# Kernel optimization log

Measured on AMD Instinct MI355X. Metric: run time of the kernel, lower is better.

The kernel has to match this reference:

```python
import jax, jax.numpy as jnp
import numpy as np
from jax import lax

B_, L_, D_ = 4, 3136, 256
DH, DS, DR = 256, 16, 16  # d_inner//2, d_state, dt_rank (ceil(256/16))


def _ln(x, g, b):
    m = x.mean(-1, keepdims=True)
    v = ((x - m) ** 2).mean(-1, keepdims=True)
    return (x - m) * lax.rsqrt(v + 1e-5) * g + b


def _dwconv_same(x, w):
    # x: (B, C, L), w: (C, 1, K) depthwise, padding='same', no bias
    return lax.conv_general_dilated(x, w, (1,), 'SAME',
        dimension_numbers=('NCH', 'OIH', 'NCH'), feature_group_count=x.shape[1])


def _selective_scan(u, delta, A, Bm, Cm, Dp, delta_bias):
    # u, delta: (b, d, l); A: (d, n); Bm, Cm: (b, n, l)
    delta = jax.nn.softplus(delta + delta_bias[None, :, None])
    dA = jnp.exp(jnp.einsum('bdl,dn->lbdn', delta, A))          # (l,b,d,n)
    dBu = jnp.einsum('bdl,bnl,bdl->lbdn', delta, Bm, u)          # (l,b,d,n)
    C_l = jnp.transpose(Cm, (2, 0, 1))                           # (l,b,n)
    h0 = jnp.zeros(dA.shape[1:], u.dtype)

    def step(h, inp):
        dA_t, dBu_t, C_t = inp
        h = dA_t * h + dBu_t
        return h, jnp.einsum('bdn,bn->bd', h, C_t)

    _, ys = lax.scan(step, h0, (dA, dBu, C_l))                   # ys: (l,b,d)
    return jnp.transpose(ys, (1, 2, 0)) + u * Dp[None, :, None]


def _mamba(x, in_proj_w, conv_x_w, conv_z_w, x_proj_w, dt_proj_w, dt_proj_b, A_log, Dp, out_proj_w):
    xz = jnp.einsum('bld,ed->bel', x, in_proj_w)                 # (b, 2*DH, l)
    xb, zb = xz[:, :DH], xz[:, DH:]
    xb = jax.nn.silu(_dwconv_same(xb, conv_x_w))
    zb = jax.nn.silu(_dwconv_same(zb, conv_z_w))
    x_dbl = jnp.einsum('bdl,ed->ble', xb, x_proj_w)              # (b, l, DR+2*DS)
    dt, Bm, Cm = x_dbl[..., :DR], x_dbl[..., DR:DR + DS], x_dbl[..., DR + DS:]
    delta = jnp.einsum('blr,dr->bdl', dt, dt_proj_w)             # (b, DH, l)
    Bm = jnp.transpose(Bm, (0, 2, 1))                            # (b, DS, l)
    Cm = jnp.transpose(Cm, (0, 2, 1))
    A = -jnp.exp(A_log)
    y = _selective_scan(xb, delta, A, Bm, Cm, Dp, dt_proj_b)     # (b, DH, l)
    y = jnp.concatenate([y, zb], axis=1)                         # (b, 2*DH, l)
    return jnp.einsum('bel,de->bld', y, out_proj_w)


def _block(x, ln1_g, ln1_b, ln2_g, ln2_b, in_proj_w, conv_x_w, conv_z_w,
           x_proj_w, dt_proj_w, dt_proj_b, A_log, Dp, out_proj_w,
           mlp_w1, mlp_b1, mlp_w2, mlp_b2):
    x = x + _mamba(_ln(x, ln1_g, ln1_b), in_proj_w, conv_x_w, conv_z_w,
                   x_proj_w, dt_proj_w, dt_proj_b, A_log, Dp, out_proj_w)
    h = _ln(x, ln2_g, ln2_b)
    h = jax.nn.gelu(jnp.einsum('bld,hd->blh', h, mlp_w1) + mlp_b1, approximate=False)
    return x + (jnp.einsum('blh,dh->bld', h, mlp_w2) + mlp_b2)


def setup_inputs() -> dict:
    key = jax.random.key(0)
    ks = jax.random.split(key, 12)
    f = lambda k, s, sc=0.02: jax.random.normal(k, s, dtype=jnp.float32) * sc
    dt = jnp.exp(jax.random.uniform(ks[9], (DH,), dtype=jnp.float32)
                 * (np.log(0.1) - np.log(0.001)) + np.log(0.001))
    dt = jnp.clip(dt, 1e-4)
    inv_dt = dt + jnp.log(-jnp.expm1(-dt))
    return {
        'x': jax.random.normal(ks[0], (B_, L_, D_), dtype=jnp.float32),
        'ln1_g': jnp.ones((D_,), jnp.float32), 'ln1_b': jnp.zeros((D_,), jnp.float32),
        'ln2_g': jnp.ones((D_,), jnp.float32), 'ln2_b': jnp.zeros((D_,), jnp.float32),
        'in_proj_w': f(ks[1], (2 * DH, D_)),
        'conv_x_w': f(ks[2], (DH, 1, 3), 0.1),
        'conv_z_w': f(ks[3], (DH, 1, 3), 0.1),
        'x_proj_w': f(ks[4], (DR + 2 * DS, DH)),
        'dt_proj_w': f(ks[5], (DH, DR), DR ** -0.5),
        'dt_proj_b': inv_dt,
        'A_log': jnp.log(jnp.tile(jnp.arange(1, DS + 1, dtype=jnp.float32)[None, :], (DH, 1))),
        'Dp': jnp.ones((DH,), jnp.float32),
        'out_proj_w': f(ks[6], (D_, 2 * DH)),
        'mlp_w1': f(ks[7], (4 * D_, D_)), 'mlp_b1': jnp.zeros((4 * D_,), jnp.float32),
        'mlp_w2': f(ks[8], (D_, 4 * D_)), 'mlp_b2': jnp.zeros((D_,), jnp.float32),
    }


def reference(x, ln1_g, ln1_b, ln2_g, ln2_b, in_proj_w, conv_x_w, conv_z_w,
              x_proj_w, dt_proj_w, dt_proj_b, A_log, Dp, out_proj_w,
              mlp_w1, mlp_b1, mlp_w2, mlp_b2):
    return _block(x, ln1_g, ln1_b, ln2_g, ln2_b, in_proj_w, conv_x_w, conv_z_w,
                  x_proj_w, dt_proj_w, dt_proj_b, A_log, Dp, out_proj_w,
                  mlp_w1, mlp_b1, mlp_w2, mlp_b2)
```

## Files before the change

kernel.cpp:

```cpp
#include <hip/hip_runtime.h>
#include <hip/hip_bf16.h>

#define B_ 4
#define L_ 3136
#define D_ 256
#define NCH 49
#define LCH 64
#define M_ (B_*L_)

__device__ __forceinline__ float bf2f(unsigned short u) {
    union { unsigned int i; float f; } v; v.i = ((unsigned int)u) << 16; return v.f;
}
__device__ __forceinline__ unsigned short f2bs(float f) {
    __hip_bfloat16 h = __float2bfloat16(f);
    return *(unsigned short*)&h;
}
__device__ __forceinline__ float ldw(const void* p, size_t i, bool bf) {
    return bf ? bf2f(((const unsigned short*)p)[i]) : ((const float*)p)[i];
}
__device__ __forceinline__ void cvt4(ushort4 a, float* o) {
    o[0] = bf2f(a.x); o[1] = bf2f(a.y); o[2] = bf2f(a.z); o[3] = bf2f(a.w);
}
__device__ __forceinline__ void cvt8g(const unsigned short* p, bool v, float* o) {
    if (v) {
        ushort4 a = *(const ushort4*)p;
        ushort4 b = *(const ushort4*)(p + 4);
        cvt4(a, o); cvt4(b, o + 4);
    } else {
        #pragma unroll
        for (int i = 0; i < 8; ++i) o[i] = 0.f;
    }
}
__device__ __forceinline__ float dpp_add_xor1(float x) {
    int m = __builtin_amdgcn_update_dpp(0, __float_as_int(x), 0xB1, 0xF, 0xF, true);
    return x + __int_as_float(m);
}
__device__ __forceinline__ float dpp_add_xor2(float x) {
    int m = __builtin_amdgcn_update_dpp(0, __float_as_int(x), 0x4E, 0xF, 0xF, true);
    return x + __int_as_float(m);
}

__global__ __launch_bounds__(256) void detect_kernel(
    const unsigned int* __restrict__ xw, int* __restrict__ flag)
{
    int t = threadIdx.x; int cnt = 0;
    for (int i = t; i < 2048; i += 256) {
        unsigned int lo = xw[i] & 0xFFFFu;
        unsigned int e = (lo >> 7) & 0xFFu;
        if (e >= 0x58u && e <= 0x97u) cnt++;
    }
    #pragma unroll
    for (int o = 32; o > 0; o >>= 1) cnt += __shfl_down(cnt, o);
    __shared__ int sred[4];
    if ((t & 63) == 0) sred[t >> 6] = cnt;
    __syncthreads();
    if (t == 0) flag[0] = (sred[0] + sred[1] + sred[2] + sred[3] > 1024) ? 1 : 0;
}

__global__ __launch_bounds__(256) void ln_kernel(
    const void* __restrict__ xin, int inmode,
    const void* __restrict__ g, const void* __restrict__ bsh,
    unsigned short* __restrict__ out, const int* __restrict__ flagp)
{
    const bool wbf = (*flagp != 0);
    const bool inbf = (inmode < 0) ? wbf : true;
    int row = blockIdx.x * 4 + (threadIdx.x >> 6);
    int lane = threadIdx.x & 63;
    size_t idx = (size_t)row * 256 + lane * 4;
    float v[4];
    if (inbf) {
        ushort4 a = *(const ushort4*)((const unsigned short*)xin + idx);
        cvt4(a, v);
    } else {
        float4 a = *(const float4*)((const float*)xin + idx);
        v[0] = a.x; v[1] = a.y; v[2] = a.z; v[3] = a.w;
    }
    float s = v[0] + v[1] + v[2] + v[3];
    float s2 = v[0]*v[0] + v[1]*v[1] + v[2]*v[2] + v[3]*v[3];
    #pragma unroll
    for (int o = 32; o > 0; o >>= 1) { s += __shfl_xor(s, o); s2 += __shfl_xor(s2, o); }
    float mean = s * (1.f / 256.f);
    float var  = s2 * (1.f / 256.f) - mean * mean;
    float rs = rsqrtf(var + 1e-5f);
    ushort4 o;
    o.x = f2bs((v[0] - mean) * rs * ldw(g, lane*4+0, wbf) + ldw(bsh, lane*4+0, wbf));
    o.y = f2bs((v[1] - mean) * rs * ldw(g, lane*4+1, wbf) + ldw(bsh, lane*4+1, wbf));
    o.z = f2bs((v[2] - mean) * rs * ldw(g, lane*4+2, wbf) + ldw(bsh, lane*4+2, wbf));
    o.w = f2bs((v[3] - mean) * rs * ldw(g, lane*4+3, wbf) + ldw(bsh, lane*4+3, wbf));
    *(ushort4*)(out + idx) = o;
}

enum { EPI_NONE = 0, EPI_SP = 1, EPI_RES = 2, EPI_GELU = 3, EPI_OUT = 4 };

typedef __attribute__((ext_vector_type(8))) short bf16x8;
typedef __attribute__((ext_vector_type(4))) float f32x4;

__device__ __forceinline__ void gload_lds16(const void* g, void* l) {
    __builtin_amdgcn_global_load_lds(
        (const __attribute__((address_space(1))) unsigned int*)g,
        (__attribute__((address_space(3))) unsigned int*)l, 16, 0, 0);
}

template<int EPI>
__global__ __launch_bounds__(256) void mgemm_kernel(
    const unsigned short* __restrict__ A, const unsigned short* __restrict__ A2, int Ksplit,
    const void* __restrict__ W, void* __restrict__ Cout,
    int N, int K, int lda, int ldc,
    const void* __restrict__ bias, const void* __restrict__ resb,
    const unsigned short* __restrict__ resf, const int* __restrict__ flagp)
{
    const bool wbf = (*flagp != 0);
    __shared__ unsigned short As[2][64][64];
    __shared__ unsigned short Ws[2][64][64];
    const int tid = threadIdx.x;

    const int nwg = gridDim.x * gridDim.y;
    int bid = blockIdx.y * gridDim.x + blockIdx.x;
    int wgid = ((nwg & 7) == 0) ? ((bid & 7) * (nwg >> 3) + (bid >> 3)) : bid;
    const int bx = wgid % gridDim.x;
    const int by = wgid / gridDim.x;
    const int bm = by * 64, bn = bx * 64;

    const int l = tid & 63, wid = tid >> 6;
    const int wr = wid >> 1, wc = wid & 1;
    const int lr = l & 15;
    const int lq = l >> 4;
    const int srow = tid >> 3;
    const int sblk = ((tid & 7) ^ (srow & 7)) * 8;
    const int dcol = (tid & 7) * 8;

    f32x4 acc[2][2] = {};
    const int NT = K >> 6;

    auto stage = [&](int buf, int k0s) {
        const unsigned short* Ab; int kc;
        if (k0s < Ksplit) { Ab = A;  kc = k0s; }
        else              { Ab = A2; kc = k0s - Ksplit; }
        gload_lds16(Ab + (size_t)(bm + srow) * lda + kc + sblk,      &As[buf][srow][dcol]);
        gload_lds16(Ab + (size_t)(bm + 32 + srow) * lda + kc + sblk, &As[buf][32 + srow][dcol]);
        if (wbf) {
            const unsigned short* Wb = (const unsigned short*)W;
            gload_lds16(Wb + (size_t)(bn + srow) * K + k0s + sblk,      &Ws[buf][srow][dcol]);
            gload_lds16(Wb + (size_t)(bn + 32 + srow) * K + k0s + sblk, &Ws[buf][32 + srow][dcol]);
        } else {
            const float* Wf = (const float*)W;
            #pragma unroll
            for (int h = 0; h < 2; ++h) {
                int row = h * 32 + srow;
                const float* p = Wf + (size_t)(bn + row) * K + k0s + (tid & 7) * 8;
                float4 w0 = *(const float4*)p;
                float4 w1 = *(const float4*)(p + 4);
                ushort4 o0, o1;
                o0.x = f2bs(w0.x); o0.y = f2bs(w0.y); o0.z = f2bs(w0.z); o0.w = f2bs(w0.w);
                o1.x = f2bs(w1.x); o1.y = f2bs(w1.y); o1.z = f2bs(w1.z); o1.w = f2bs(w1.w);
                *(ushort4*)&Ws[buf][row][sblk]     = o0;
                *(ushort4*)&Ws[buf][row][sblk + 4] = o1;
            }
        }
    };

    stage(0, 0);
    asm volatile("s_waitcnt vmcnt(0)" ::: "memory");
    __syncthreads();

    int cur = 0;
    for (int kt = 0; kt < NT; ++kt) {
        if (kt + 1 < NT) stage(cur ^ 1, (kt + 1) << 6);

        bf16x8 af[2][2], bfr[2][2];
        #pragma unroll
        for (int i = 0; i < 2; ++i) {
            #pragma unroll
            for (int ks = 0; ks < 2; ++ks) {
                int ca = ((ks * 4 + lq) ^ (lr & 7)) * 8;
                af[i][ks]  = *(const bf16x8*)&As[cur][wr * 32 + i * 16 + lr][ca];
                bfr[i][ks] = *(const bf16x8*)&Ws[cur][wc * 32 + i * 16 + lr][ca];
            }
        }
        #pragma unroll
        for (int ks = 0; ks < 2; ++ks)
            #pragma unroll
            for (int i = 0; i < 2; ++i)
                #pragma unroll
                for (int j = 0; j < 2; ++j)
                    acc[i][j] = __builtin_amdgcn_mfma_f32_16x16x32_bf16(af[i][ks], bfr[j][ks], acc[i][j], 0, 0, 0);

        if (kt + 1 < NT) {
            asm volatile("s_waitcnt vmcnt(0)" ::: "memory");
            __syncthreads();
            cur ^= 1;
        }
    }

    #pragma unroll
    for (int i = 0; i < 2; ++i) {
        #pragma unroll
        for (int j = 0; j < 2; ++j) {
            const int col = bn + wc * 32 + j * 16 + lr;
            #pragma unroll
            for (int e = 0; e < 4; ++e) {
                const int row = bm + wr * 32 + i * 16 + lq * 4 + e;
                float t = acc[i][j][e];
                if (EPI == EPI_RES) {
                    t += ldw(resb, (size_t)row * 256 + col, wbf);
                } else if (EPI == EPI_GELU) {
                    t += ldw(bias, col, wbf);
                    t = 0.5f * t * (1.f + erff(t * 0.70710678118654752f));
                } else if (EPI == EPI_OUT) {
                    t += ldw(bias, col, wbf) + bf2f(resf[(size_t)row * 256 + col]);
                }
                if (EPI == EPI_OUT && !wbf) {
                    ((float*)Cout)[(size_t)row * ldc + col] = t;
                } else {
                    ((unsigned short*)Cout)[(size_t)row * ldc + col] = f2bs(t);
                }
            }
        }
    }
}

__global__ __launch_bounds__(256) void xproj_kernel(
    const unsigned short* __restrict__ A, const void* __restrict__ W,
    float* __restrict__ Cout, const int* __restrict__ flagp)
{
    const bool wbf = (*flagp != 0);
    __shared__ unsigned short As[2][64][64];
    __shared__ unsigned short Ws[2][64][64];
    const int tid = threadIdx.x;
    const int bm = blockIdx.y * 64;

    const int l = tid & 63, wid = tid >> 6;
    const int wr = wid >> 1, wc = wid & 1;
    const int lr = l & 15, lq = l >> 4;
    const int srow = tid >> 3;
    const int sblk = ((tid & 7) ^ (srow & 7)) * 8;
    const int dcol = (tid & 7) * 8;

    {
        ushort4 zz4; zz4.x = 0; zz4.y = 0; zz4.z = 0; zz4.w = 0;
        int buf = tid >> 7, rr = 48 + ((tid >> 3) & 15), cc = (tid & 7) * 8;
        *(ushort4*)&Ws[buf][rr][cc] = zz4;
        *(ushort4*)&Ws[buf][rr][cc + 4] = zz4;
    }
    __syncthreads();

    f32x4 acc[2][2] = {};

    auto stage = [&](int buf, int k0s) {
        gload_lds16(A + (size_t)(bm + srow) * 256 + k0s + sblk,      &As[buf][srow][dcol]);
        gload_lds16(A + (size_t)(bm + 32 + srow) * 256 + k0s + sblk, &As[buf][32 + srow][dcol]);
        if (wbf) {
            const unsigned short* Wb = (const unsigned short*)W;
            gload_lds16(Wb + (size_t)srow * 256 + k0s + sblk, &Ws[buf][srow][dcol]);
            if (srow < 16)
                gload_lds16(Wb + (size_t)(32 + srow) * 256 + k0s + sblk, &Ws[buf][32 + srow][dcol]);
        } else {
            const float* Wf = (const float*)W;
            #pragma unroll
            for (int h = 0; h < 2; ++h) {
                int row = h * 32 + srow;
                if (row < 48) {
                    const float* p = Wf + (size_t)row * 256 + k0s + (tid & 7) * 8;
                    float4 w0 = *(const float4*)p;
                    float4 w1 = *(const float4*)(p + 4);
                    ushort4 o0, o1;
                    o0.x = f2bs(w0.x); o0.y = f2bs(w0.y); o0.z = f2bs(w0.z); o0.w = f2bs(w0.w);
                    o1.x = f2bs(w1.x); o1.y = f2bs(w1.y); o1.z = f2bs(w1.z); o1.w = f2bs(w1.w);
                    *(ushort4*)&Ws[buf][row][sblk]     = o0;
                    *(ushort4*)&Ws[buf][row][sblk + 4] = o1;
                }
            }
        }
    };

    stage(0, 0);
    asm volatile("s_waitcnt vmcnt(0)" ::: "memory");
    __syncthreads();

    int cur = 0;
    for (int kt = 0; kt < 4; ++kt) {
        if (kt + 1 < 4) stage(cur ^ 1, (kt + 1) << 6);
        bf16x8 af[2][2], bfr[2][2];
        #pragma unroll
        for (int i = 0; i < 2; ++i) {
            #pragma unroll
            for (int ks = 0; ks < 2; ++ks) {
                int ca = ((ks * 4 + lq) ^ (lr & 7)) * 8;
                af[i][ks]  = *(const bf16x8*)&As[cur][wr * 32 + i * 16 + lr][ca];
                bfr[i][ks] = *(const bf16x8*)&Ws[cur][wc * 32 + i * 16 + lr][ca];
            }
        }
        #pragma unroll
        for (int ks = 0; ks < 2; ++ks)
            #pragma unroll
            for (int i = 0; i < 2; ++i)
                #pragma unroll
                for (int j = 0; j < 2; ++j)
                    acc[i][j] = __builtin_amdgcn_mfma_f32_16x16x32_bf16(af[i][ks], bfr[j][ks], acc[i][j], 0, 0, 0);
        if (kt + 1 < 4) {
            asm volatile("s_waitcnt vmcnt(0)" ::: "memory");
            __syncthreads();
            cur ^= 1;
        }
    }

    #pragma unroll
    for (int i = 0; i < 2; ++i) {
        #pragma unroll
        for (int j = 0; j < 2; ++j) {
            const int col = wc * 32 + j * 16 + lr;
            if (col < 48) {
                #pragma unroll
                for (int e = 0; e < 4; ++e) {
                    const int row = bm + wr * 32 + i * 16 + lq * 4 + e;
                    Cout[(size_t)row * 48 + col] = acc[i][j][e];
                }
            }
        }
    }
}

__global__ __launch_bounds__(256) void dtgemm_kernel(
    const float* __restrict__ Axd, const void* __restrict__ W,
    unsigned short* __restrict__ Cout, const void* __restrict__ bias,
    const int* __restrict__ flagp)
{
    const bool wbf = (*flagp != 0);
    __shared__ unsigned short Ah[64][16];
    __shared__ unsigned short Al[64][16];
    __shared__ unsigned short Wb[64][16];
    const int tid = threadIdx.x;
    const int nwg = gridDim.x * gridDim.y;
    int bid = blockIdx.y * gridDim.x + blockIdx.x;
    int wgid = ((nwg & 7) == 0) ? ((bid & 7) * (nwg >> 3) + (bid >> 3)) : bid;
    const int bx = wgid % gridDim.x, by = wgid / gridDim.x;
    const int bm = by * 64, bn = bx * 64;

    {
        int rr = tid >> 2, cc = (tid & 3) * 4;
        float4 v = *(const float4*)(Axd + (size_t)(bm + rr) * 48 + cc);
        float vv[4] = {v.x, v.y, v.z, v.w};
        ushort4 hi4, lo4;
        unsigned short* hp = (unsigned short*)&hi4;
        unsigned short* lp = (unsigned short*)&lo4;
        #pragma unroll
        for (int j = 0; j < 4; ++j) {
            unsigned short h = f2bs(vv[j]);
            hp[j] = h;
            lp[j] = f2bs(vv[j] - bf2f(h));
        }
        *(ushort4*)&Ah[rr][cc] = hi4;
        *(ushort4*)&Al[rr][cc] = lo4;
        ushort4 wb4;
        unsigned short* wp = (unsigned short*)&wb4;
        if (wbf) {
            wb4 = *(const ushort4*)((const unsigned short*)W + (size_t)(bn + rr) * 16 + cc);
        } else {
            float4 wv = *(const float4*)((const float*)W + (size_t)(bn + rr) * 16 + cc);
            wp[0] = f2bs(wv.x); wp[1] = f2bs(wv.y); wp[2] = f2bs(wv.z); wp[3] = f2bs(wv.w);
        }
        *(ushort4*)&Wb[rr][cc] = wb4;
    }
    __syncthreads();

    const int l = tid & 63, wid = tid >> 6;
    const int wr = wid >> 1, wc = wid & 1;
    const int lr = l & 15, lq = l >> 4;

    f32x4 acc[2][2] = {};
    bf16x8 ah[2], al8[2], wb8[2];
    #pragma unroll
    for (int i = 0; i < 2; ++i) { ah[i] = bf16x8{}; al8[i] = bf16x8{}; wb8[i] = bf16x8{}; }
    if (lq < 2) {
        #pragma unroll
        for (int i = 0; i < 2; ++i) {
            ah[i]  = *(const bf16x8*)&Ah[wr * 32 + i * 16 + lr][lq * 8];
            al8[i] = *(const bf16x8*)&Al[wr * 32 + i * 16 + lr][lq * 8];
            wb8[i] = *(const bf16x8*)&Wb[wc * 32 + i * 16 + lr][lq * 8];
        }
    }
    #pragma unroll
    for (int i = 0; i < 2; ++i)
        #pragma unroll
        for (int j = 0; j < 2; ++j) {
            acc[i][j] = __builtin_amdgcn_mfma_f32_16x16x32_bf16(ah[i],  wb8[j], acc[i][j], 0, 0, 0);
            acc[i][j] = __builtin_amdgcn_mfma_f32_16x16x32_bf16(al8[i], wb8[j], acc[i][j], 0, 0, 0);
        }

    #pragma unroll
    for (int i = 0; i < 2; ++i) {
        #pragma unroll
        for (int j = 0; j < 2; ++j) {
            const int col = bn + wc * 32 + j * 16 + lr;
            #pragma unroll
            for (int e = 0; e < 4; ++e) {
                const int row = bm + wr * 32 + i * 16 + lq * 4 + e;
                float t = acc[i][j][e] + ldw(bias, col, wbf);
                t = (t > 20.f) ? t : log1pf(__expf(t));
                Cout[(size_t)row * 256 + col] = f2bs(t);
            }
        }
    }
}

__global__ __launch_bounds__(256) void conv_silu_kernel(
    const unsigned short* __restrict__ xz,
    const void* __restrict__ wx, const void* __restrict__ wz,
    unsigned short* __restrict__ u, unsigned short* __restrict__ z,
    const int* __restrict__ flagp)
{
    const bool wbf = (*flagp != 0);
    int sub = threadIdx.x >> 5;
    int cb = (threadIdx.x & 31) * 8;
    int bl = blockIdx.x * 8 + sub;
    int l = bl % L_;
    const unsigned short* r = xz + (size_t)bl * 512;
    bool hasm = (l > 0), hasp = (l < L_ - 1);

    float wxa[24], wza[24];
    if (wbf) {
        const unsigned short* px = (const unsigned short*)wx + 3 * cb;
        const unsigned short* pz = (const unsigned short*)wz + 3 * cb;
        #pragma unroll
        for (int t = 0; t < 3; ++t) {
            cvt4(*(const ushort4*)(px + t * 8), &wxa[t * 8]);
            cvt4(*(const ushort4*)(px + t * 8 + 4), &wxa[t * 8 + 4]);
            cvt4(*(const ushort4*)(pz + t * 8), &wza[t * 8]);
            cvt4(*(const ushort4*)(pz + t * 8 + 4), &wza[t * 8 + 4]);
        }
    } else {
        const float* px = (const float*)wx + 3 * cb;
        const float* pz = (const float*)wz + 3 * cb;
        #pragma unroll
        for (int t = 0; t < 6; ++t) {
            *(float4*)&wxa[t * 4] = *(const float4*)(px + t * 4);
            *(float4*)&wza[t * 4] = *(const float4*)(pz + t * 4);
        }
    }

    float xm[8], xc[8], xp[8];
    cvt8g(r + cb - 512, hasm, xm);
    cvt8g(r + cb,       true, xc);
    cvt8g(r + cb + 512, hasp, xp);
    ushort4 o0, o1;
    {
        unsigned short* op = (unsigned short*)&o0;
        unsigned short* op1 = (unsigned short*)&o1;
        #pragma unroll
        for (int j = 0; j < 8; ++j) {
            float v = xm[j] * wxa[3 * j] + xc[j] * wxa[3 * j + 1] + xp[j] * wxa[3 * j + 2];
            v = v / (1.f + __expf(-v));
            if (j < 4) op[j] = f2bs(v); else op1[j - 4] = f2bs(v);
        }
    }
    *(ushort4*)(u + (size_t)bl * 256 + cb) = o0;
    *(ushort4*)(u + (size_t)bl * 256 + cb + 4) = o1;

    cvt8g(r + cb - 256,  hasm, xm);
    cvt8g(r + 256 + cb,  true, xc);
    cvt8g(r + 768 + cb,  hasp, xp);
    {
        unsigned short* op = (unsigned short*)&o0;
        unsigned short* op1 = (unsigned short*)&o1;
        #pragma unroll
        for (int j = 0; j < 8; ++j) {
            float v = xm[j] * wza[3 * j] + xc[j] * wza[3 * j + 1] + xp[j] * wza[3 * j + 2];
            v = v / (1.f + __expf(-v));
            if (j < 4) op[j] = f2bs(v); else op1[j - 4] = f2bs(v);
        }
    }
    *(ushort4*)(z + (size_t)bl * 256 + cb) = o0;
    *(ushort4*)(z + (size_t)bl * 256 + cb + 4) = o1;
}

__global__ __launch_bounds__(256) void scan_a_kernel(
    const unsigned short* __restrict__ delta, const unsigned short* __restrict__ u,
    const float* __restrict__ xdbl, const void* __restrict__ A_log,
    float* __restrict__ hend, float* __restrict__ dsum, const int* __restrict__ flagp)
{
    const bool wbf = (*flagp != 0);
    int blk = blockIdx.x;
    int b = blk / (NCH * 16);
    int rem = blk % (NCH * 16);
    int c = rem / 16, db = rem % 16;

    __shared__ unsigned int sduT[16][68];
    __shared__ float sBT[16][68];

    const unsigned short* dp = delta + (size_t)b * L_ * 256;
    const unsigned short* up = u     + (size_t)b * L_ * 256;
    const float* xd = xdbl + (size_t)b * L_ * 48;

    int r = threadIdx.x >> 2, q = (threadIdx.x & 3) * 4;
    int lrow = c * 64 + r;
    {
        ushort4 dv = *(const ushort4*)(dp + (size_t)lrow * 256 + db * 16 + q);
        ushort4 uv = *(const ushort4*)(up + (size_t)lrow * 256 + db * 16 + q);
        sduT[q + 0][r] = (unsigned)dv.x | ((unsigned)uv.x << 16);
        sduT[q + 1][r] = (unsigned)dv.y | ((unsigned)uv.y << 16);
        sduT[q + 2][r] = (unsigned)dv.z | ((unsigned)uv.z << 16);
        sduT[q + 3][r] = (unsigned)dv.w | ((unsigned)uv.w << 16);
        float4 Bv = *(const float4*)(xd + (size_t)lrow * 48 + 16 + q);
        sBT[q + 0][r] = Bv.x; sBT[q + 1][r] = Bv.y;
        sBT[q + 2][r] = Bv.z; sBT[q + 3][r] = Bv.w;
    }
    __syncthreads();

    int g = threadIdx.x >> 4, n = threadIdx.x & 15;
    int d = db * 16 + g;
    float An2 = -__expf(ldw(A_log, d * 16 + n, wbf)) * 1.44269504088896f;
    float h = 0.f, s = 0.f;
    #pragma unroll 4
    for (int tb = 0; tb < 16; ++tb) {
        uint4 du4 = *(const uint4*)&sduT[g][tb * 4];
        float4 B4 = *(const float4*)&sBT[n][tb * 4];
        #pragma unroll
        for (int j = 0; j < 4; ++j) {
            unsigned du = (j == 0) ? du4.x : (j == 1) ? du4.y : (j == 2) ? du4.z : du4.w;
            float Bn = (j == 0) ? B4.x : (j == 1) ? B4.y : (j == 2) ? B4.z : B4.w;
            float ds = __uint_as_float(du << 16);
            float ut = __uint_as_float(du & 0xFFFF0000u);
            float e = exp2f(ds * An2);
            h = fmaf(e, h, ds * ut * Bn);
            s += ds;
        }
    }
    size_t pair = (size_t)b * 256 + d;
    hend[(pair * NCH + c) * 16 + n] = h;
    if (n == 0) dsum[pair * NCH + c] = s;
}

__global__ __launch_bounds__(64) void scan_b_kernel(
    const void* __restrict__ A_log, float* __restrict__ hend,
    const float* __restrict__ dsum, const int* __restrict__ flagp)
{
    const bool wbf = (*flagp != 0);
    int gid = blockIdx.x * 64 + threadIdx.x;
    int pair = gid >> 4, n = gid & 15;
    int d = pair & 255;
    float An = -__expf(ldw(A_log, d * 16 + n, wbf));
    float H = 0.f;
    #pragma unroll 1
    for (int c0 = 0; c0 < NCH; c0 += 7) {
        float he[7], dd[7];
        #pragma unroll
        for (int j = 0; j < 7; ++j) {
            he[j] = hend[((size_t)pair * NCH + c0 + j) * 16 + n];
            dd[j] = dsum[(size_t)pair * NCH + c0 + j];
        }
        #pragma unroll
        for (int j = 0; j < 7; ++j) {
            hend[((size_t)pair * NCH + c0 + j) * 16 + n] = H;
            H = __expf(An * dd[j]) * H + he[j];
        }
    }
}

__global__ __launch_bounds__(256) void scan_c_kernel(
    const unsigned short* __restrict__ delta, const unsigned short* __restrict__ u,
    const float* __restrict__ xdbl, const void* __restrict__ A_log,
    const void* __restrict__ Dp, const float* __restrict__ hinit,
    unsigned short* __restrict__ y, const int* __restrict__ flagp)
{
    const bool wbf = (*flagp != 0);
    int blk = blockIdx.x;
    int b = blk / (NCH * 16);
    int rem = blk % (NCH * 16);
    int c = rem / 16, db = rem % 16;

    __shared__ unsigned int sduT[16][68];
    __shared__ float sBCT[16][132];
    __shared__ float sypT[16][4][68];
    __shared__ unsigned short sy[64][16];

    const unsigned short* dp = delta + (size_t)b * L_ * 256;
    const unsigned short* up = u     + (size_t)b * L_ * 256;
    const float* xd = xdbl + (size_t)b * L_ * 48;

    int r = threadIdx.x >> 2, q = (threadIdx.x & 3) * 4;
    int lrow = c * 64 + r;
    {
        ushort4 dv = *(const ushort4*)(dp + (size_t)lrow * 256 + db * 16 + q);
        ushort4 uv = *(const ushort4*)(up + (size_t)lrow * 256 + db * 16 + q);
        sduT[q + 0][r] = (unsigned)dv.x | ((unsigned)uv.x << 16);
        sduT[q + 1][r] = (unsigned)dv.y | ((unsigned)uv.y << 16);
        sduT[q + 2][r] = (unsigned)dv.z | ((unsigned)uv.z << 16);
        sduT[q + 3][r] = (unsigned)dv.w | ((unsigned)uv.w << 16);
        float4 Bv = *(const float4*)(xd + (size_t)lrow * 48 + 16 + q);
        float4 Cv = *(const float4*)(xd + (size_t)lrow * 48 + 32 + q);
        float2 t0; t0.x = Bv.x; t0.y = Cv.x; *(float2*)&sBCT[q + 0][r * 2] = t0;
        float2 t1; t1.x = Bv.y; t1.y = Cv.y; *(float2*)&sBCT[q + 1][r * 2] = t1;
        float2 t2; t2.x = Bv.z; t2.y = Cv.z; *(float2*)&sBCT[q + 2][r * 2] = t2;
        float2 t3; t3.x = Bv.w; t3.y = Cv.w; *(float2*)&sBCT[q + 3][r * 2] = t3;
    }
    __syncthreads();

    int g = threadIdx.x >> 4, n = threadIdx.x & 15;
    int d = db * 16 + g;
    float An2 = -__expf(ldw(A_log, d * 16 + n, wbf)) * 1.44269504088896f;
    size_t pair = (size_t)b * 256 + d;
    float h = hinit[(pair * NCH + c) * 16 + n];
    const bool wlane = ((n & 3) == 0);
    const int p = n >> 2;
    #pragma unroll 4
    for (int tb = 0; tb < 16; ++tb) {
        uint4 du4 = *(const uint4*)&sduT[g][tb * 4];
        float4 bc01 = *(const float4*)&sBCT[n][tb * 8];
        float4 bc23 = *(const float4*)&sBCT[n][tb * 8 + 4];
        float yp4[4];
        #pragma unroll
        for (int j = 0; j < 4; ++j) {
            unsigned du = (j == 0) ? du4.x : (j == 1) ? du4.y : (j == 2) ? du4.z : du4.w;
            float Bn = (j == 0) ? bc01.x : (j == 1) ? bc01.z : (j == 2) ? bc23.x : bc23.z;
            float Cn = (j == 0) ? bc01.y : (j == 1) ? bc01.w : (j == 2) ? bc23.y : bc23.w;
            float ds = __uint_as_float(du << 16);
            float ut = __uint_as_float(du & 0xFFFF0000u);
            float e = exp2f(ds * An2);
            h = fmaf(e, h, ds * ut * Bn);
            float yp = h * Cn;
            yp = dpp_add_xor1(yp);
            yp = dpp_add_xor2(yp);
            yp4[j] = yp;
        }
        if (wlane) *(float4*)&sypT[g][p][tb * 4] = *(float4*)yp4;
    }
    __syncthreads();

    #pragma unroll
    for (int cc = 0; cc < 4; ++cc) {
        int cell = threadIdx.x + cc * 256;
        int t2 = cell >> 4, gg = cell & 15;
        float sum = sypT[gg][0][t2] + sypT[gg][1][t2] + sypT[gg][2][t2] + sypT[gg][3][t2];
        unsigned du = sduT[gg][t2];
        float ut = __uint_as_float(du & 0xFFFF0000u);
        float Dd = ldw(Dp, db * 16 + gg, wbf);
        sy[t2][gg] = f2bs(sum + ut * Dd);
    }
    __syncthreads();
    *(ushort4*)(y + ((size_t)b * L_ + c * 64 + r) * 256 + db * 16 + q) = *(ushort4*)&sy[r][q];
}

extern "C" void kernel_launch(void* const* d_in, const int* in_sizes, int n_in,
                              void* d_out, int out_size, void* d_ws, size_t ws_size,
                              hipStream_t stream) {
    const void* x         = d_in[0];
    const void* ln1_g     = d_in[1];
    const void* ln1_b     = d_in[2];
    const void* ln2_g     = d_in[3];
    const void* ln2_b     = d_in[4];
    const void* in_proj_w = d_in[5];
    const void* conv_x_w  = d_in[6];
    const void* conv_z_w  = d_in[7];
    const void* x_proj_w  = d_in[8];
    const void* dt_proj_w = d_in[9];
    const void* dt_proj_b = d_in[10];
    const void* A_log     = d_in[11];
    const void* Dp        = d_in[12];
    const void* out_proj_w= d_in[13];
    const void* mlp_w1    = d_in[14];
    const void* mlp_b1    = d_in[15];
    const void* mlp_w2    = d_in[16];
    const void* mlp_b2    = d_in[17];

    float* ws = (float*)d_ws;
    unsigned short* xz    = (unsigned short*)(ws);
    unsigned short* delta = (unsigned short*)(ws);
    unsigned short* yb    = (unsigned short*)(ws + 1605632);
    float*          xdbl  = ws + 3211264;
    float*          hend  = ws + 3813376;
    float*          dsum  = ws + 4616192;
    unsigned short* hmid  = (unsigned short*)(ws);
    unsigned short* ub    = (unsigned short*)(ws + 6422528);
    unsigned short* xres  = (unsigned short*)(ws + 6422528);
    unsigned short* xnb   = (unsigned short*)(ws + 8028160);
    int*            flag  = (int*)(ws + 9633792);

    dim3 blk(256);
    const int KNOSPLIT = 1 << 30;

    detect_kernel<<<1, blk, 0, stream>>>((const unsigned int*)x, flag);

    ln_kernel<<<M_ / 4, blk, 0, stream>>>(x, -1, ln1_g, ln1_b, xnb, flag);

    mgemm_kernel<EPI_NONE><<<dim3(8, 196), blk, 0, stream>>>(
        xnb, nullptr, KNOSPLIT, in_proj_w, xz, 512, 256, 256, 512, nullptr, nullptr, nullptr, flag);

    conv_silu_kernel<<<M_ / 8, blk, 0, stream>>>(xz, conv_x_w, conv_z_w, ub, xnb, flag);

    xproj_kernel<<<dim3(1, 196), blk, 0, stream>>>(ub, x_proj_w, xdbl, flag);

    dtgemm_kernel<<<dim3(4, 196), blk, 0, stream>>>(xdbl, dt_proj_w, delta, dt_proj_b, flag);

    scan_a_kernel<<<B_ * NCH * 16, blk, 0, stream>>>(delta, ub, xdbl, A_log, hend, dsum, flag);
    scan_b_kernel<<<256, dim3(64), 0, stream>>>(A_log, hend, dsum, flag);
    scan_c_kernel<<<B_ * NCH * 16, blk, 0, stream>>>(delta, ub, xdbl, A_log, Dp, hend, yb, flag);

    mgemm_kernel<EPI_RES><<<dim3(4, 196), blk, 0, stream>>>(
        yb, xnb, 256, out_proj_w, xres, 256, 512, 256, 256, nullptr, x, nullptr, flag);

    ln_kernel<<<M_ / 4, blk, 0, stream>>>(xres, 1, ln2_g, ln2_b, xnb, flag);

    mgemm_kernel<EPI_GELU><<<dim3(16, 196), blk, 0, stream>>>(
        xnb, nullptr, KNOSPLIT, mlp_w1, hmid, 1024, 256, 256, 1024, mlp_b1, nullptr, nullptr, flag);

    mgemm_kernel<EPI_OUT><<<dim3(4, 196), blk, 0, stream>>>(
        hmid, nullptr, KNOSPLIT, mlp_w2, d_out, 256, 1024, 1024, 256, mlp_b2, nullptr, xres, flag);
}
```

Baseline: 296.7 us.

## Fold chunk-carry scan into scan_c and halve xproj row tile

```diff
diff --git a/kernel.cpp b/kernel.cpp
--- a/kernel.cpp
+++ b/kernel.cpp
@@ -224,13 +224,12 @@
     float* __restrict__ Cout, const int* __restrict__ flagp)
 {
     const bool wbf = (*flagp != 0);
-    __shared__ unsigned short As[2][64][64];
+    __shared__ unsigned short As[2][32][64];
     __shared__ unsigned short Ws[2][64][64];
     const int tid = threadIdx.x;
-    const int bm = blockIdx.y * 64;
+    const int bm = blockIdx.y * 32;
 
     const int l = tid & 63, wid = tid >> 6;
-    const int wr = wid >> 1, wc = wid & 1;
     const int lr = l & 15, lq = l >> 4;
     const int srow = tid >> 3;
     const int sblk = ((tid & 7) ^ (srow & 7)) * 8;
@@ -244,11 +243,10 @@
     }
     __syncthreads();
 
-    f32x4 acc[2][2] = {};
+    f32x4 acc[2] = {};
 
     auto stage = [&](int buf, int k0s) {
-        gload_lds16(A + (size_t)(bm + srow) * 256 + k0s + sblk,      &As[buf][srow][dcol]);
-        gload_lds16(A + (size_t)(bm + 32 + srow) * 256 + k0s + sblk, &As[buf][32 + srow][dcol]);
+        gload_lds16(A + (size_t)(bm + srow) * 256 + k0s + sblk, &As[buf][srow][dcol]);
         if (wbf) {
             const unsigned short* Wb = (const unsigned short*)W;
             gload_lds16(Wb + (size_t)srow * 256 + k0s + sblk, &Ws[buf][srow][dcol]);
@@ -280,23 +278,19 @@
     int cur = 0;
     for (int kt = 0; kt < 4; ++kt) {
         if (kt + 1 < 4) stage(cur ^ 1, (kt + 1) << 6);
-        bf16x8 af[2][2], bfr[2][2];
-        #pragma unroll
-        for (int i = 0; i < 2; ++i) {
-            #pragma unroll
-            for (int ks = 0; ks < 2; ++ks) {
-                int ca = ((ks * 4 + lq) ^ (lr & 7)) * 8;
-                af[i][ks]  = *(const bf16x8*)&As[cur][wr * 32 + i * 16 + lr][ca];
-                bfr[i][ks] = *(const bf16x8*)&Ws[cur][wc * 32 + i * 16 + lr][ca];
-            }
+        bf16x8 af[2][2], bfr[2];
+        #pragma unroll
+        for (int ks = 0; ks < 2; ++ks) {
+            int ca = ((ks * 4 + lq) ^ (lr & 7)) * 8;
+            af[0][ks] = *(const bf16x8*)&As[cur][lr][ca];
+            af[1][ks] = *(const bf16x8*)&As[cur][16 + lr][ca];
+            bfr[ks]   = *(const bf16x8*)&Ws[cur][wid * 16 + lr][ca];
         }
         #pragma unroll
         for (int ks = 0; ks < 2; ++ks)
             #pragma unroll
             for (int i = 0; i < 2; ++i)
-                #pragma unroll
-                for (int j = 0; j < 2; ++j)
-                    acc[i][j] = __builtin_amdgcn_mfma_f32_16x16x32_bf16(af[i][ks], bfr[j][ks], acc[i][j], 0, 0, 0);
+                acc[i] = __builtin_amdgcn_mfma_f32_16x16x32_bf16(af[i][ks], bfr[ks], acc[i], 0, 0, 0);
         if (kt + 1 < 4) {
             asm volatile("s_waitcnt vmcnt(0)" ::: "memory");
             __syncthreads();
@@ -304,19 +298,15 @@
         }
     }
 
-    #pragma unroll
-    for (int i = 0; i < 2; ++i) {
-        #pragma unroll
-        for (int j = 0; j < 2; ++j) {
-            const int col = wc * 32 + j * 16 + lr;
-            if (col < 48) {
-                #pragma unroll
-                for (int e = 0; e < 4; ++e) {
-                    const int row = bm + wr * 32 + i * 16 + lq * 4 + e;
-                    Cout[(size_t)row * 48 + col] = acc[i][j][e];
-                }
-            }
-        }
+    const int col = wid * 16 + lr;
+    if (col < 48) {
+        #pragma unroll
+        for (int i = 0; i < 2; ++i)
+            #pragma unroll
+            for (int e = 0; e < 4; ++e) {
+                const int row = bm + i * 16 + lq * 4 + e;
+                Cout[(size_t)row * 48 + col] = acc[i][e];
+            }
     }
 }
 
@@ -530,36 +520,11 @@
     if (n == 0) dsum[pair * NCH + c] = s;
 }
 
-__global__ __launch_bounds__(64) void scan_b_kernel(
-    const void* __restrict__ A_log, float* __restrict__ hend,
-    const float* __restrict__ dsum, const int* __restrict__ flagp)
-{
-    const bool wbf = (*flagp != 0);
-    int gid = blockIdx.x * 64 + threadIdx.x;
-    int pair = gid >> 4, n = gid & 15;
-    int d = pair & 255;
-    float An = -__expf(ldw(A_log, d * 16 + n, wbf));
-    float H = 0.f;
-    #pragma unroll 1
-    for (int c0 = 0; c0 < NCH; c0 += 7) {
-        float he[7], dd[7];
-        #pragma unroll
-        for (int j = 0; j < 7; ++j) {
-            he[j] = hend[((size_t)pair * NCH + c0 + j) * 16 + n];
-            dd[j] = dsum[(size_t)pair * NCH + c0 + j];
-        }
-        #pragma unroll
-        for (int j = 0; j < 7; ++j) {
-            hend[((size_t)pair * NCH + c0 + j) * 16 + n] = H;
-            H = __expf(An * dd[j]) * H + he[j];
-        }
-    }
-}
-
 __global__ __launch_bounds__(256) void scan_c_kernel(
     const unsigned short* __restrict__ delta, const unsigned short* __restrict__ u,
     const float* __restrict__ xdbl, const void* __restrict__ A_log,
-    const void* __restrict__ Dp, const float* __restrict__ hinit,
+    const void* __restrict__ Dp, const float* __restrict__ hend,
+    const float* __restrict__ dsum,
     unsigned short* __restrict__ y, const int* __restrict__ flagp)
 {
     const bool wbf = (*flagp != 0);
@@ -599,7 +564,27 @@
     int d = db * 16 + g;
     float An2 = -__expf(ldw(A_log, d * 16 + n, wbf)) * 1.44269504088896f;
     size_t pair = (size_t)b * 256 + d;
-    float h = hinit[(pair * NCH + c) * 16 + n];
+
+    float h = 0.f;
+    {
+        size_t base = pair * NCH;
+        for (int c0 = 0; c0 < c; c0 += 8) {
+            float he[8], dd[8];
+            #pragma unroll
+            for (int j = 0; j < 8; ++j) {
+                int cc2 = c0 + j;
+                bool ok = (cc2 < c);
+                he[j] = ok ? hend[(base + cc2) * 16 + n] : 0.f;
+                dd[j] = ok ? dsum[base + cc2] : 0.f;
+            }
+            #pragma unroll
+            for (int j = 0; j < 8; ++j) {
+                if (c0 + j < c)
+                    h = exp2f(An2 * dd[j]) * h + he[j];
+            }
+        }
+    }
+
     const bool wlane = ((n & 3) == 0);
     const int p = n >> 2;
     #pragma unroll 4
@@ -687,13 +672,12 @@
 
     conv_silu_kernel<<<M_ / 8, blk, 0, stream>>>(xz, conv_x_w, conv_z_w, ub, xnb, flag);
 
-    xproj_kernel<<<dim3(1, 196), blk, 0, stream>>>(ub, x_proj_w, xdbl, flag);
+    xproj_kernel<<<dim3(1, 392), blk, 0, stream>>>(ub, x_proj_w, xdbl, flag);
 
     dtgemm_kernel<<<dim3(4, 196), blk, 0, stream>>>(xdbl, dt_proj_w, delta, dt_proj_b, flag);
 
     scan_a_kernel<<<B_ * NCH * 16, blk, 0, stream>>>(delta, ub, xdbl, A_log, hend, dsum, flag);
-    scan_b_kernel<<<256, dim3(64), 0, stream>>>(A_log, hend, dsum, flag);
-    scan_c_kernel<<<B_ * NCH * 16, blk, 0, stream>>>(delta, ub, xdbl, A_log, Dp, hend, yb, flag);
+    scan_c_kernel<<<B_ * NCH * 16, blk, 0, stream>>>(delta, ub, xdbl, A_log, Dp, hend, dsum, yb, flag);
 
     mgemm_kernel<EPI_RES><<<dim3(4, 196), blk, 0, stream>>>(
         yb, xnb, 256, out_proj_w, xres, 256, 512, 256, 256, nullptr, x, nullptr, flag);
```

After: 298.4 us. Within noise of the previous version (+0.6%).
